# Optimization experiments

Measured on AMD Instinct MI355X. Metric: run time of the kernel, lower is better.

The kernel has to match this reference:

```python
import jax, jax.numpy as jnp
import numpy as np

HIDDEN = 256        # hidden width of the dynamics MLP
N_ODE_STEPS = 2     # fixed-step RK4 steps over t_sim = [0, 1] per block


def setup_inputs() -> dict:
    key = jax.random.key(0)
    ks = jax.random.split(key, 8)
    S, B, N, d, p, block = 2, 8, 2048, 64, 32, 8
    s = jax.random.normal(ks[0], (S, B, N, d), jnp.float32)
    # strictly increasing time grid so delta = diff(t) > 0
    dt_raw = jax.random.uniform(ks[1], (S, B, block + 1), jnp.float32)
    t = jnp.cumsum(0.05 + 0.1 * dt_raw, axis=2)
    Phi = jax.random.normal(ks[2], (S, B, N, p), jnp.float32)
    b = 0.1 * jax.random.normal(ks[3], (S, B, N, d), jnp.float32)
    W1 = jax.random.normal(ks[4], (d + p, HIDDEN), jnp.float32) / np.sqrt(d + p).astype(np.float32)
    b1 = jnp.zeros((HIDDEN,), jnp.float32)
    W2 = jax.random.normal(ks[5], (HIDDEN, d), jnp.float32) / np.sqrt(HIDDEN).astype(np.float32)
    b2 = jnp.zeros((d,), jnp.float32)
    return dict(s=s, t=t, Phi=Phi, b=b, W1=W1, b1=b1, W2=W2, b2=b2)


def _dyn(x, Phi, b, W1, b1, W2, b2):
    # f(t, x, Phi, b): MLP over per-node latent + spatial features, plus forcing b.
    h = jnp.tanh(jnp.einsum('sbnf,fh->sbnh', jnp.concatenate([x, Phi], axis=-1), W1) + b1)
    return jnp.einsum('sbnh,hd->sbnd', h, W2) + b2 + b


def reference(s, t, Phi, b, W1, b1, W2, b2):
    S, B, N, d = s.shape
    block = t.shape[2] - 1
    delta = jnp.diff(t, axis=2)                      # (S, B, block)
    deltas = jnp.moveaxis(delta, 2, 0)[..., None, None]  # (block, S, B, 1, 1)
    dt = 1.0 / N_ODE_STEPS

    def g(x, dlt):
        # scaled dynamics: f(t, x, Phi, b) * delta  (time-rescaled to [0, 1])
        return _dyn(x, Phi, b, W1, b1, W2, b2) * dlt

    def block_step(x, dlt):
        def rk4(x, _):
            k1 = g(x, dlt)
            k2 = g(x + 0.5 * dt * k1, dlt)
            k3 = g(x + 0.5 * dt * k2, dlt)
            k4 = g(x + dt * k3, dlt)
            return x + (dt / 6.0) * (k1 + 2.0 * k2 + 2.0 * k3 + k4), None
        x, _ = jax.lax.scan(rk4, x, None, length=N_ODE_STEPS)
        return x, x

    _, s_stack = jax.lax.scan(block_step, s, deltas)  # (block, S, B, N, d)
    # 'S B block N d -> S (B block) N d'
    return jnp.moveaxis(s_stack, 0, 2).reshape(S, B * block, N, d)
```

## Files before the change

kernel.cpp:

```cpp
#include <hip/hip_runtime.h>

typedef short  short8   __attribute__((ext_vector_type(8)));
typedef float  floatx4  __attribute__((ext_vector_type(4)));
typedef unsigned int uintx2 __attribute__((ext_vector_type(2)));

#define LOG2E_X2 2.8853900817779268f

__device__ __forceinline__ float tanh_pre(float y) {
    float e = __builtin_amdgcn_exp2f(y);
    return 1.0f - 2.0f * __builtin_amdgcn_rcpf(1.0f + e);
}

__device__ __forceinline__ unsigned short bf16rne(float f) {
    unsigned u = __float_as_uint(f);
    u += 0x7FFFu + ((u >> 16) & 1u);
    return (unsigned short)(u >> 16);
}

#if __has_builtin(__builtin_amdgcn_cvt_pk_bf16_f32)
__device__ __forceinline__ unsigned pk2(float a, float b) {
    auto r = __builtin_amdgcn_cvt_pk_bf16_f32(a, b);
    unsigned u; __builtin_memcpy(&u, &r, 4);
    return u;
}
#else
__device__ __forceinline__ unsigned pk2(float a, float b) {
    unsigned r;
    asm("v_cvt_pk_bf16_f32 %0, %1, %2" : "=v"(r) : "v"(a), "v"(b));
    return r;
}
#endif

__device__ __forceinline__ floatx4 unpk4(uintx2 u) {
    floatx4 r;
    r[0] = __uint_as_float(u.x << 16);
    r[1] = __uint_as_float(u.x & 0xffff0000u);
    r[2] = __uint_as_float(u.y << 16);
    r[3] = __uint_as_float(u.y & 0xffff0000u);
    return r;
}

__global__ __launch_bounds__(512, 4) void ode_mfma(
    const float* __restrict__ s_in,  const float* __restrict__ t_in,
    const float* __restrict__ phi_in,const float* __restrict__ bfr_in,
    const float* __restrict__ w1_in, const float* __restrict__ b1_in,
    const float* __restrict__ w2_in, const float* __restrict__ b2_in,
    float* __restrict__ out)
{
    const int tid  = threadIdx.x;
    const int w    = tid >> 6;
    const int lane = tid & 63;
    const int l15  = lane & 15;
    const int q    = lane >> 4;
    const int wg   = blockIdx.x;
    const int sb   = wg >> 5;
    const int n0   = (wg & 31) << 6;
    const int rowg0 = sb * 2048 + n0;

    __shared__ __align__(16) unsigned short Atile[64][104];
    __shared__ __align__(16) unsigned short Hs[64][264];
    __shared__ float dls[8];

    {
        int row = tid >> 3, cc = tid & 7;
        floatx4 p = *(const floatx4*)(phi_in + (rowg0 + row) * 32 + cc * 4);
        uintx2 px = { pk2(p[0], p[1]), pk2(p[2], p[3]) };
        *(uintx2*)&Atile[row][64 + cc * 4] = px;
    }
    if (tid < 8) dls[tid] = t_in[sb * 9 + tid + 1] - t_in[sb * 9 + tid];

#define DO_G1(RT0)                                                              \
    {                                                                           \
        floatx4 acc1[4][2];                                                     \
        {                                                                       \
            short8 xb[2];                                                       \
            _Pragma("unroll")                                                   \
            for (int r2 = 0; r2 < 2; ++r2)                                      \
                xb[r2] = *(const short8*)&Atile[(RT0 + r2) * 16 + l15][q * 8];  \
            _Pragma("unroll")                                                   \
            for (int ht = 0; ht < 4; ++ht)                                      \
                _Pragma("unroll")                                               \
                for (int r2 = 0; r2 < 2; ++r2)                                  \
                    acc1[ht][r2] = __builtin_amdgcn_mfma_f32_16x16x32_bf16(     \
                        w1f[ht][0], xb[r2], bbf[ht], 0, 0, 0);                  \
        }                                                                       \
        _Pragma("unroll")                                                       \
        for (int kk = 1; kk < 3; ++kk) {                                        \
            short8 xb[2];                                                       \
            _Pragma("unroll")                                                   \
            for (int r2 = 0; r2 < 2; ++r2)                                      \
                xb[r2] = *(const short8*)&Atile[(RT0 + r2) * 16 + l15][kk * 32 + q * 8]; \
            _Pragma("unroll")                                                   \
            for (int ht = 0; ht < 4; ++ht)                                      \
                _Pragma("unroll")                                               \
                for (int r2 = 0; r2 < 2; ++r2)                                  \
                    acc1[ht][r2] = __builtin_amdgcn_mfma_f32_16x16x32_bf16(     \
                        w1f[ht][kk], xb[r2], acc1[ht][r2], 0, 0, 0);            \
        }                                                                       \
        _Pragma("unroll")                                                       \
        for (int ht = 0; ht < 4; ++ht)                                          \
            _Pragma("unroll")                                                   \
            for (int r2 = 0; r2 < 2; ++r2) {                                    \
                uintx2 hp = { pk2(tanh_pre(acc1[ht][r2][0]), tanh_pre(acc1[ht][r2][1])), \
                              pk2(tanh_pre(acc1[ht][r2][2]), tanh_pre(acc1[ht][r2][3])) }; \
                *(uintx2*)&Hs[(RT0 + r2) * 16 + l15][hb0 + ht * 16 + q * 4] = hp; \
            }                                                                   \
    }

#define DO_G2(SI)                                                               \
    {                                                                           \
        const int rt = (SI) * 2 + rt_rel;                                       \
        const unsigned short* hrow = &Hs[rt * 16 + l15][0];                     \
        floatx4 acc2a, acc2b;                                                   \
        {                                                                       \
            short8 hb = *(const short8*)&hrow[q * 8];                           \
            acc2a = __builtin_amdgcn_mfma_f32_16x16x32_bf16(                    \
                w2f[0][0], hb, unpk4(fpk[SI][0]), 0, 0, 0);                     \
            acc2b = __builtin_amdgcn_mfma_f32_16x16x32_bf16(                    \
                w2f[1][0], hb, unpk4(fpk[SI][1]), 0, 0, 0);                     \
        }                                                                       \
        _Pragma("unroll")                                                       \
        for (int kk = 1; kk < 8; ++kk) {                                        \
            short8 hb = *(const short8*)&hrow[kk * 32 + q * 8];                 \
            acc2a = __builtin_amdgcn_mfma_f32_16x16x32_bf16(                    \
                w2f[0][kk], hb, acc2a, 0, 0, 0);                                \
            acc2b = __builtin_amdgcn_mfma_f32_16x16x32_bf16(                    \
                w2f[1][kk], hb, acc2b, 0, 0, 0);                                \
        }                                                                       \
        _Pragma("unroll")                                                       \
        for (int h = 0; h < 2; ++h) {                                           \
            floatx4 kv = (h == 0 ? acc2a : acc2b) * dlt;                        \
            floatx4 xe;                                                         \
            if (sub == 0)      { kacc[SI][h] = kv;            xe = xv[SI][h] + 0.25f * kv; } \
            else if (sub == 1) { kacc[SI][h] += 2.0f * kv;    xe = xv[SI][h] + 0.25f * kv; } \
            else if (sub == 2) { kacc[SI][h] += 2.0f * kv;    xe = xv[SI][h] + 0.5f  * kv; } \
            else               { xv[SI][h] += (kacc[SI][h] + kv) * (1.0f / 12.0f); xe = xv[SI][h]; } \
            uintx2 px = { pk2(xe[0], xe[1]), pk2(xe[2], xe[3]) };               \
            *(uintx2*)&Atile[rt * 16 + l15][dp + h * 16 + q * 4] = px;          \
        }                                                                       \
        if (ii == 7) {                                                          \
            const size_t ob = (size_t)((sb * 8 + blk) * 2048 + n0 + rt * 16 + l15) * 64; \
            _Pragma("unroll")                                                   \
            for (int h = 0; h < 2; ++h)                                         \
                *(floatx4*)(out + ob + dp + h * 16 + q * 4) = xv[SI][h];        \
        }                                                                       \
    }

    if (w < 4) {
        const int hb0 = w * 64;
        short8 w1f[4][3];
#pragma unroll
        for (int ht = 0; ht < 4; ++ht)
#pragma unroll
            for (int kk = 0; kk < 3; ++kk) {
                short8 f;
#pragma unroll
                for (int j = 0; j < 8; ++j) {
                    int k = kk * 32 + q * 8 + j;
                    int hc = hb0 + ht * 16 + l15;
                    f[j] = (short)bf16rne(w1_in[k * 256 + hc] * LOG2E_X2);
                }
                w1f[ht][kk] = f;
            }
        floatx4 bbf[4];
#pragma unroll
        for (int ht = 0; ht < 4; ++ht) {
            floatx4 v = *(const floatx4*)(b1_in + hb0 + ht * 16 + q * 4);
            bbf[ht] = v * LOG2E_X2;
        }

        __syncthreads();
        DO_G1(0)
#pragma unroll 1
        for (int it = 0; it < 64; ++it) {
            __syncthreads();
            DO_G1(2)
            __syncthreads();
            if (it < 63) { DO_G1(0) }
        }
    } else {
        const int g = w - 4;
        const int rt_rel = g >> 1;
        const int dp = (g & 1) * 32;
        short8 w2f[2][8];
#pragma unroll
        for (int h = 0; h < 2; ++h)
#pragma unroll
            for (int kk = 0; kk < 8; ++kk) {
                short8 f;
#pragma unroll
                for (int j = 0; j < 8; ++j) {
                    int k = kk * 32 + q * 8 + j;
                    f[j] = (short)bf16rne(w2_in[k * 64 + dp + h * 16 + l15]);
                }
                w2f[h][kk] = f;
            }

        floatx4 xv[2][2], kacc[2][2];
        uintx2 fpk[2][2];
#pragma unroll
        for (int si = 0; si < 2; ++si) {
            const int rt = si * 2 + rt_rel;
            const int rg = rowg0 + rt * 16 + l15;
#pragma unroll
            for (int h = 0; h < 2; ++h) {
                const int dh = dp + h * 16 + q * 4;
                xv[si][h] = *(const floatx4*)(s_in + rg * 64 + dh);
                floatx4 fb = *(const floatx4*)(b2_in + dh)
                           + *(const floatx4*)(bfr_in + rg * 64 + dh);
                fpk[si][h] = (uintx2){ pk2(fb[0], fb[1]), pk2(fb[2], fb[3]) };
                uintx2 px = { pk2(xv[si][h][0], xv[si][h][1]),
                              pk2(xv[si][h][2], xv[si][h][3]) };
                *(uintx2*)&Atile[rt * 16 + l15][dh] = px;
            }
        }

        __syncthreads();
#pragma unroll 1
        for (int blk = 0; blk < 8; ++blk) {
            const float dlt = dls[blk];
#pragma unroll 1
            for (int ii = 0; ii < 8; ++ii) {
                const int sub = ii & 3;
                __syncthreads();
                DO_G2(0)
                __syncthreads();
                DO_G2(1)
            }
        }
    }
#undef DO_G1
#undef DO_G2
}

extern "C" void kernel_launch(void* const* d_in, const int* in_sizes, int n_in,
                              void* d_out, int out_size, void* d_ws, size_t ws_size,
                              hipStream_t stream) {
    const float* s_in  = (const float*)d_in[0];
    const float* t_in  = (const float*)d_in[1];
    const float* phi   = (const float*)d_in[2];
    const float* bfr   = (const float*)d_in[3];
    const float* w1    = (const float*)d_in[4];
    const float* b1    = (const float*)d_in[5];
    const float* w2    = (const float*)d_in[6];
    const float* b2    = (const float*)d_in[7];
    ode_mfma<<<512, 512, 0, stream>>>(s_in, t_in, phi, bfr, w1, b1, w2, b2, (float*)d_out);
}
```

Baseline: 298.3 us.

## Interleave GEMM1 MFMA with tanh per hidden tile, stagger block starts, raise producer priority

Restructures the first-layer GEMM so each hidden tile's MFMA chain is followed immediately by its tanh and bf16 store to shared memory. This lets transcendental and LDS work overlap with later MFMA tiles instead of running only after all MFMAs finish. All A-tile fragments are loaded up front, and the producer waves raise their scheduling priority so the GEMM1 stage is not starved by the GEMM2 waves. Every other group of 256 blocks sleeps briefly at start to stagger phases across CUs. This adds some register pressure and a small fixed delay for half the blocks.

```diff
diff --git a/kernel.cpp b/kernel.cpp
--- a/kernel.cpp
+++ b/kernel.cpp
@@ -47,6 +47,8 @@
     const float* __restrict__ w2_in, const float* __restrict__ b2_in,
     float* __restrict__ out)
 {
+    if ((blockIdx.x >> 8) & 1) __builtin_amdgcn_s_sleep(37);
+
     const int tid  = threadIdx.x;
     const int w    = tid >> 6;
     const int lane = tid & 63;
@@ -71,40 +73,33 @@
 
 #define DO_G1(RT0)                                                              \
     {                                                                           \
-        floatx4 acc1[4][2];                                                     \
-        {                                                                       \
-            short8 xb[2];                                                       \
+        short8 xb[3][2];                                                        \
+        _Pragma("unroll")                                                       \
+        for (int kk = 0; kk < 3; ++kk)                                          \
             _Pragma("unroll")                                                   \
             for (int r2 = 0; r2 < 2; ++r2)                                      \
-                xb[r2] = *(const short8*)&Atile[(RT0 + r2) * 16 + l15][q * 8];  \
-            _Pragma("unroll")                                                   \
-            for (int ht = 0; ht < 4; ++ht)                                      \
-                _Pragma("unroll")                                               \
-                for (int r2 = 0; r2 < 2; ++r2)                                  \
-                    acc1[ht][r2] = __builtin_amdgcn_mfma_f32_16x16x32_bf16(     \
-                        w1f[ht][0], xb[r2], bbf[ht], 0, 0, 0);                  \
-        }                                                                       \
-        _Pragma("unroll")                                                       \
-        for (int kk = 1; kk < 3; ++kk) {                                        \
-            short8 xb[2];                                                       \
-            _Pragma("unroll")                                                   \
-            for (int r2 = 0; r2 < 2; ++r2)                                      \
-                xb[r2] = *(const short8*)&Atile[(RT0 + r2) * 16 + l15][kk * 32 + q * 8]; \
-            _Pragma("unroll")                                                   \
-            for (int ht = 0; ht < 4; ++ht)                                      \
-                _Pragma("unroll")                                               \
-                for (int r2 = 0; r2 < 2; ++r2)                                  \
-                    acc1[ht][r2] = __builtin_amdgcn_mfma_f32_16x16x32_bf16(     \
-                        w1f[ht][kk], xb[r2], acc1[ht][r2], 0, 0, 0);            \
-        }                                                                       \
-        _Pragma("unroll")                                                       \
-        for (int ht = 0; ht < 4; ++ht)                                          \
-            _Pragma("unroll")                                                   \
-            for (int r2 = 0; r2 < 2; ++r2) {                                    \
-                uintx2 hp = { pk2(tanh_pre(acc1[ht][r2][0]), tanh_pre(acc1[ht][r2][1])), \
-                              pk2(tanh_pre(acc1[ht][r2][2]), tanh_pre(acc1[ht][r2][3])) }; \
-                *(uintx2*)&Hs[(RT0 + r2) * 16 + l15][hb0 + ht * 16 + q * 4] = hp; \
-            }                                                                   \
+                xb[kk][r2] = *(const short8*)&Atile[(RT0 + r2) * 16 + l15][kk * 32 + q * 8]; \
+        _Pragma("unroll")                                                       \
+        for (int ht = 0; ht < 4; ++ht) {                                        \
+            floatx4 a0 = __builtin_amdgcn_mfma_f32_16x16x32_bf16(               \
+                w1f[ht][0], xb[0][0], bbf[ht], 0, 0, 0);                        \
+            floatx4 a1 = __builtin_amdgcn_mfma_f32_16x16x32_bf16(               \
+                w1f[ht][0], xb[0][1], bbf[ht], 0, 0, 0);                        \
+            a0 = __builtin_amdgcn_mfma_f32_16x16x32_bf16(                       \
+                w1f[ht][1], xb[1][0], a0, 0, 0, 0);                             \
+            a1 = __builtin_amdgcn_mfma_f32_16x16x32_bf16(                       \
+                w1f[ht][1], xb[1][1], a1, 0, 0, 0);                             \
+            a0 = __builtin_amdgcn_mfma_f32_16x16x32_bf16(                       \
+                w1f[ht][2], xb[2][0], a0, 0, 0, 0);                             \
+            a1 = __builtin_amdgcn_mfma_f32_16x16x32_bf16(                       \
+                w1f[ht][2], xb[2][1], a1, 0, 0, 0);                             \
+            uintx2 hp0 = { pk2(tanh_pre(a0[0]), tanh_pre(a0[1])),               \
+                           pk2(tanh_pre(a0[2]), tanh_pre(a0[3])) };             \
+            *(uintx2*)&Hs[(RT0 + 0) * 16 + l15][hb0 + ht * 16 + q * 4] = hp0;   \
+            uintx2 hp1 = { pk2(tanh_pre(a1[0]), tanh_pre(a1[1])),               \
+                           pk2(tanh_pre(a1[2]), tanh_pre(a1[3])) };             \
+            *(uintx2*)&Hs[(RT0 + 1) * 16 + l15][hb0 + ht * 16 + q * 4] = hp1;   \
+        }                                                                       \
     }
 
 #define DO_G2(SI)                                                               \
@@ -168,6 +163,8 @@
             floatx4 v = *(const floatx4*)(b1_in + hb0 + ht * 16 + q * 4);
             bbf[ht] = v * LOG2E_X2;
         }
+
+        __builtin_amdgcn_s_setprio(1);
 
         __syncthreads();
         DO_G1(0)
```

Measured after the change: 354.5 us. +18.8%, slower.

## Offload half of tanh activation work from GEMM1 waves to GEMM2 waves

Applied to the files above, without the earlier changes.

The GEMM1 waves now apply tanh and bf16 packing to only half of their hidden accumulators. The other half goes as raw fp32 into a new shared Raw buffer, and the GEMM2 waves run tanh on it and write it into Hs before their MFMA pass. The aim is to balance the transcendental work between the two wave groups, since the GEMM1 side appears to be the critical path. In exchange it doubles the number of block-wide barriers per stage and adds extra LDS traffic and shared memory use, which may lower occupancy.

```diff
diff --git a/kernel.cpp b/kernel.cpp
--- a/kernel.cpp
+++ b/kernel.cpp
@@ -59,6 +59,7 @@
 
     __shared__ __align__(16) unsigned short Atile[64][104];
     __shared__ __align__(16) unsigned short Hs[64][264];
+    __shared__ __align__(16) float Raw[2][32][132];
     __shared__ float dls[8];
 
     {
@@ -69,7 +70,7 @@
     }
     if (tid < 8) dls[tid] = t_in[sb * 9 + tid + 1] - t_in[sb * 9 + tid];
 
-#define DO_G1(RT0)                                                              \
+#define DO_G1P(RT0, S)                                                          \
     {                                                                           \
         floatx4 acc1[4][2];                                                     \
         {                                                                       \
@@ -98,13 +99,32 @@
                         w1f[ht][kk], xb[r2], acc1[ht][r2], 0, 0, 0);            \
         }                                                                       \
         _Pragma("unroll")                                                       \
-        for (int ht = 0; ht < 4; ++ht)                                          \
+        for (int ht = 0; ht < 2; ++ht)                                          \
             _Pragma("unroll")                                                   \
             for (int r2 = 0; r2 < 2; ++r2) {                                    \
                 uintx2 hp = { pk2(tanh_pre(acc1[ht][r2][0]), tanh_pre(acc1[ht][r2][1])), \
                               pk2(tanh_pre(acc1[ht][r2][2]), tanh_pre(acc1[ht][r2][3])) }; \
                 *(uintx2*)&Hs[(RT0 + r2) * 16 + l15][hb0 + ht * 16 + q * 4] = hp; \
             }                                                                   \
+        _Pragma("unroll")                                                       \
+        for (int ht = 2; ht < 4; ++ht)                                          \
+            _Pragma("unroll")                                                   \
+            for (int r2 = 0; r2 < 2; ++r2)                                      \
+                *(floatx4*)&Raw[S][r2 * 16 + l15][(hb0 >> 1) + (ht - 2) * 16 + q * 4] = acc1[ht][r2]; \
+    }
+
+#define DO_HELP(S)                                                              \
+    {                                                                           \
+        const int hrow = (S) * 32 + rt_rel * 16 + l15;                          \
+        _Pragma("unroll")                                                       \
+        for (int k = 0; k < 4; ++k) {                                           \
+            const int c = dp * 2 + q * 16 + k * 4;                              \
+            floatx4 v = *(const floatx4*)&Raw[S][rt_rel * 16 + l15][c];         \
+            uintx2 hp = { pk2(tanh_pre(v[0]), tanh_pre(v[1])),                  \
+                          pk2(tanh_pre(v[2]), tanh_pre(v[3])) };                \
+            const int g = ((c >> 5) << 6) + 32 + (c & 31);                      \
+            *(uintx2*)&Hs[hrow][g] = hp;                                        \
+        }                                                                       \
     }
 
 #define DO_G2(SI)                                                               \
@@ -170,18 +190,20 @@
         }
 
         __syncthreads();
-        DO_G1(0)
+        DO_G1P(0, 0)
 #pragma unroll 1
         for (int it = 0; it < 64; ++it) {
             __syncthreads();
-            DO_G1(2)
-            __syncthreads();
-            if (it < 63) { DO_G1(0) }
+            DO_G1P(2, 1)
+            __syncthreads();
+            __syncthreads();
+            if (it < 63) { DO_G1P(0, 0) }
+            __syncthreads();
         }
     } else {
-        const int g = w - 4;
-        const int rt_rel = g >> 1;
-        const int dp = (g & 1) * 32;
+        const int g2 = w - 4;
+        const int rt_rel = g2 >> 1;
+        const int dp = (g2 & 1) * 32;
         short8 w2f[2][8];
 #pragma unroll
         for (int h = 0; h < 2; ++h)
@@ -223,13 +245,18 @@
             for (int ii = 0; ii < 8; ++ii) {
                 const int sub = ii & 3;
                 __syncthreads();
+                DO_HELP(0)
+                __syncthreads();
                 DO_G2(0)
                 __syncthreads();
+                DO_HELP(1)
+                __syncthreads();
                 DO_G2(1)
             }
         }
     }
-#undef DO_G1
+#undef DO_G1P
+#undef DO_HELP
 #undef DO_G2
 }
 
```

New measurement: 459.4 us. 1.54x slower.
